# Performance work log

Measured on AMD Instinct MI355X. Metric: run time of the kernel, lower is better.

## Reference

```python
import jax, jax.numpy as jnp
import numpy as np

ALPHA = 0.2  # LeakyReLU negative slope
B, N, F_IN, F_OUT = 8, 2048, 256, 64


def setup_inputs() -> dict:
    key = jax.random.key(0)
    k1, k2, k3, k4 = jax.random.split(key, 4)
    x = jax.random.normal(k1, (B, N, F_IN), dtype=jnp.float32)
    adj = jax.random.randint(k2, (B, N, N), 0, 2, dtype=jnp.int32)
    # xavier_uniform with gain=1.414
    gain = 1.414
    lim_W = gain * np.sqrt(6.0 / (F_IN + F_OUT))
    W = jax.random.uniform(k3, (F_IN, F_OUT), dtype=jnp.float32, minval=-lim_W, maxval=lim_W)
    lim_a = gain * np.sqrt(6.0 / (2 * F_OUT + 1))
    a = jax.random.uniform(k4, (2 * F_OUT, 1), dtype=jnp.float32, minval=-lim_a, maxval=lim_a)
    return {"x": x, "adj": adj, "W": W, "a": a}


def reference(x, adj, W, a):
    h = jnp.einsum('bni,io->bno', x, W)  # [B, N, F_OUT]
    f_out = W.shape[1]
    # additive score a^T [h_i ; h_j] = (h_i . a_left) + (h_j . a_right)
    a_left = a[:f_out, 0]   # [F_OUT]
    a_right = a[f_out:, 0]  # [F_OUT]
    e_l = h @ a_left   # [B, N]
    e_r = h @ a_right  # [B, N]
    e = e_l[:, :, None] + e_r[:, None, :]          # [B, N, N]
    e = jnp.where(e > 0, e, ALPHA * e)             # LeakyReLU
    e = jnp.where(adj > 0, e, jnp.float32(-9e15))  # adjacency mask
    attention = jax.nn.softmax(e, axis=2)          # [B, N, N]
    h_prime = jnp.einsum('bnm,bmo->bno', attention, h)  # [B, N, F_OUT]
    return jax.nn.elu(h_prime)
```

## Files before the change

### kernel.cpp

```cpp
#include <hip/hip_runtime.h>
#include <math.h>

#define BATCH 8
#define NN 2048
#define FIN 256
#define FOUT 64
#define ALPHA 0.2f

typedef __attribute__((ext_vector_type(8))) short bf16x8;
typedef __attribute__((ext_vector_type(4))) float f32x4;

static __device__ __forceinline__ unsigned short f2bf(float f) {
  unsigned int u = __float_as_uint(f);
  u += 0x7fffu + ((u >> 16) & 1u);
  return (unsigned short)(u >> 16);
}
static __device__ __forceinline__ float bf2f(unsigned short h) {
  return __uint_as_float(((unsigned int)h) << 16);
}

__global__ __launch_bounds__(256) void k1_h(
    const float* __restrict__ x, const float* __restrict__ W,
    const float* __restrict__ a, float* __restrict__ el,
    float* __restrict__ er, unsigned char* __restrict__ hS) {
  __shared__ __align__(16) unsigned short lds[32768];
  const int t = threadIdx.x;
  const int wv = t >> 6;
  const int l = t & 63;
  const int l15 = l & 15;
  const int kg = l >> 4;

  {
    const float4* W4 = (const float4*)W;
    #pragma unroll
    for (int i = 0; i < 16; ++i) {
      int f = t + i * 256;
      float4 v = W4[f];
      int k = f >> 4;
      int ob = (f & 15) * 4;
      float vv[4] = {v.x, v.y, v.z, v.w};
      #pragma unroll
      for (int c = 0; c < 4; ++c) {
        int o = ob + c;
        unsigned short hi = f2bf(vv[c]);
        unsigned short lo = f2bf(vv[c] - bf2f(hi));
        int idx = o * 256 + (((k >> 3) ^ (o & 7)) * 8) + (k & 7);
        lds[idx] = hi;
        lds[16384 + idx] = lo;
      }
    }
  }
  __syncthreads();

  const int row = blockIdx.x * 64 + wv * 16 + l15;
  f32x4 acc[4] = {{0.f,0.f,0.f,0.f},{0.f,0.f,0.f,0.f},
                  {0.f,0.f,0.f,0.f},{0.f,0.f,0.f,0.f}};
  const float* xrow = x + (size_t)row * FIN;

  #pragma unroll
  for (int ks = 0; ks < 8; ++ks) {
    int k0 = ks * 32;
    float4 xa = *(const float4*)(xrow + k0 + kg * 8);
    float4 xb = *(const float4*)(xrow + k0 + kg * 8 + 4);
    float xv[8] = {xa.x, xa.y, xa.z, xa.w, xb.x, xb.y, xb.z, xb.w};
    bf16x8 ahi, alo;
    #pragma unroll
    for (int j = 0; j < 8; ++j) {
      unsigned short hi = f2bf(xv[j]);
      unsigned short lo = f2bf(xv[j] - bf2f(hi));
      ahi[j] = (short)hi;
      alo[j] = (short)lo;
    }
    int kgidx = ks * 4 + kg;
    #pragma unroll
    for (int ot = 0; ot < 4; ++ot) {
      int o = ot * 16 + l15;
      int base = o * 256 + ((kgidx ^ (o & 7)) * 8);
      bf16x8 bhi = *(const bf16x8*)&lds[base];
      bf16x8 blo = *(const bf16x8*)&lds[16384 + base];
      acc[ot] = __builtin_amdgcn_mfma_f32_16x16x32_bf16(ahi, bhi, acc[ot], 0, 0, 0);
      acc[ot] = __builtin_amdgcn_mfma_f32_16x16x32_bf16(ahi, blo, acc[ot], 0, 0, 0);
      acc[ot] = __builtin_amdgcn_mfma_f32_16x16x32_bf16(alo, bhi, acc[ot], 0, 0, 0);
    }
  }

  float aLv[4], aRv[4];
  #pragma unroll
  for (int ot = 0; ot < 4; ++ot) {
    aLv[ot] = a[ot * 16 + l15];
    aRv[ot] = a[64 + ot * 16 + l15];
  }
  #pragma unroll
  for (int jj = 0; jj < 4; ++jj) {
    float pl = 0.f, pr = 0.f;
    #pragma unroll
    for (int ot = 0; ot < 4; ++ot) {
      pl += acc[ot][jj] * aLv[ot];
      pr += acc[ot][jj] * aRv[ot];
    }
    #pragma unroll
    for (int s = 1; s < 16; s <<= 1) {
      pl += __shfl_xor(pl, s);
      pr += __shfl_xor(pr, s);
    }
    if (l15 == 0) {
      int grow = blockIdx.x * 64 + wv * 16 + kg * 4 + jj;
      el[grow] = pl;
      er[grow] = pr;
    }
  }

  __syncthreads();
  #pragma unroll
  for (int ot = 0; ot < 4; ++ot) {
    int o = ot * 16 + l15;
    int xorv = (o >> 1) & 3;
    #pragma unroll
    for (int jj = 0; jj < 4; ++jj) {
      int m_loc = wv * 16 + kg * 4 + jj;
      int ks2 = m_loc >> 5;
      int kg2 = (m_loc >> 3) & 3;
      int j = m_loc & 7;
      int kgp = kg2 ^ xorv;
      float v = acc[ot][jj];
      unsigned short hi = f2bf(v);
      unsigned short lo = f2bf(v - bf2f(hi));
      int base = ((ks2 * 2 + 0) * 64 + o) * 32 + kgp * 8 + j;
      lds[base] = hi;
      lds[base + 2048] = lo;
    }
  }
  __syncthreads();

  {
    const uint4* src = (const uint4*)(const void*)lds;
    uint4* dst = (uint4*)(hS + (size_t)blockIdx.x * 16384);
    #pragma unroll
    for (int i = 0; i < 4; ++i) dst[t + i * 256] = src[t + i * 256];
  }
}

__global__ __launch_bounds__(256, 3) void k2_attn(
    const int* __restrict__ adj, const unsigned char* __restrict__ hS,
    const float* __restrict__ el, const float* __restrict__ er,
    float* __restrict__ out) {
  __shared__ __align__(16) float cb[3 * 64 * 20];
  const int t = threadIdx.x;
  const int wv = t >> 6;
  const int l = t & 63;
  const int l15 = l & 15;
  const int kg = l >> 4;

  int bid = blockIdx.x;
  int swz = (bid & 7) * 128 + (bid >> 3);
  int b = swz >> 7;
  int n0 = (swz & 127) * 16;

  const int row = n0 + l15;
  const float eL = el[b * NN + row];
  const int* arow = adj + (size_t)b * NN * NN + (size_t)row * NN + wv * 512;
  const float* erp = er + b * NN + wv * 512;
  const unsigned char* hW = hS + (size_t)b * 32 * 16384 + (size_t)wv * 16 * 8192;
  const int laneoff = l15 * 64 + ((kg ^ ((l >> 1) & 3)) * 16);

  f32x4 acc[4] = {{0.f,0.f,0.f,0.f},{0.f,0.f,0.f,0.f},
                  {0.f,0.f,0.f,0.f},{0.f,0.f,0.f,0.f}};
  float S = 0.f;

  int4 av[3][2];
  float4 evc0, evc1, evn0, evn1;

  av[0][0] = *(const int4*)(arow + kg * 8);
  av[0][1] = *(const int4*)(arow + kg * 8 + 4);
  av[1][0] = *(const int4*)(arow + 32 + kg * 8);
  av[1][1] = *(const int4*)(arow + 32 + kg * 8 + 4);
  evc0 = *(const float4*)(erp + kg * 8);
  evc1 = *(const float4*)(erp + kg * 8 + 4);

  #pragma unroll
  for (int c = 0; c < 16; ++c) {
    bf16x8 curH[4], curL[4];
    {
      const unsigned char* p_ = hW + (size_t)c * 8192 + laneoff;
      #pragma unroll
      for (int ot = 0; ot < 4; ++ot) {
        curH[ot] = *(const bf16x8*)(p_ + ot * 1024);
        curL[ot] = *(const bf16x8*)(p_ + ot * 1024 + 4096);
      }
    }
    if (c < 14) {
      int mb = (c + 2) * 32;
      av[(c + 2) % 3][0] = *(const int4*)(arow + mb + kg * 8);
      av[(c + 2) % 3][1] = *(const int4*)(arow + mb + kg * 8 + 4);
    }
    if (c < 15) {
      evn0 = *(const float4*)(erp + (c + 1) * 32 + kg * 8);
      evn1 = *(const float4*)(erp + (c + 1) * 32 + kg * 8 + 4);
    }

    const int sl = c % 3;
    int a0[8] = {av[sl][0].x, av[sl][0].y, av[sl][0].z, av[sl][0].w,
                 av[sl][1].x, av[sl][1].y, av[sl][1].z, av[sl][1].w};
    float ee[8] = {evc0.x, evc0.y, evc0.z, evc0.w,
                   evc1.x, evc1.y, evc1.z, evc1.w};

    bf16x8 afh, afl;
    #pragma unroll
    for (int j = 0; j < 8; ++j) {
      float e0 = eL + ee[j];
      e0 = fmaxf(e0, ALPHA * e0);
      float w0 = (a0[j] > 0) ? __expf(e0) : 0.f;
      unsigned short h0 = f2bf(w0);
      float w0h = bf2f(h0);
      unsigned short l0 = f2bf(w0 - w0h);
      afh[j] = (short)h0;
      afl[j] = (short)l0;
      S += w0h + bf2f(l0);
    }

    #pragma unroll
    for (int ot = 0; ot < 4; ++ot) {
      acc[ot] = __builtin_amdgcn_mfma_f32_16x16x32_bf16(afh, curH[ot], acc[ot], 0, 0, 0);
      acc[ot] = __builtin_amdgcn_mfma_f32_16x16x32_bf16(afh, curL[ot], acc[ot], 0, 0, 0);
      acc[ot] = __builtin_amdgcn_mfma_f32_16x16x32_bf16(afl, curH[ot], acc[ot], 0, 0, 0);
    }

    if (c < 15) { evc0 = evn0; evc1 = evn1; }
  }

  S += __shfl_xor(S, 16);
  S += __shfl_xor(S, 32);

  __syncthreads();
  if (wv > 0) {
    float* dst = cb + ((wv - 1) * 64 + l) * 20;
    #pragma unroll
    for (int ot = 0; ot < 4; ++ot) *(f32x4*)(dst + ot * 4) = acc[ot];
    dst[16] = S;
  }
  __syncthreads();
  if (wv != 0) return;

  #pragma unroll
  for (int p = 0; p < 3; ++p) {
    const float* src = cb + (p * 64 + l) * 20;
    #pragma unroll
    for (int ot = 0; ot < 4; ++ot) acc[ot] += *(const f32x4*)(src + ot * 4);
    S += src[16];
  }

  float Sj[4];
  #pragma unroll
  for (int jj = 0; jj < 4; ++jj) Sj[jj] = __shfl(S, kg * 4 + jj);
  #pragma unroll
  for (int ot = 0; ot < 4; ++ot) {
    #pragma unroll
    for (int jj = 0; jj < 4; ++jj) {
      float v = acc[ot][jj] / Sj[jj];
      float r = v > 0.f ? v : expm1f(v);
      out[((size_t)b * NN + n0 + kg * 4 + jj) * FOUT + ot * 16 + l15] = r;
    }
  }
}

extern "C" void kernel_launch(void* const* d_in, const int* in_sizes, int n_in,
                              void* d_out, int out_size, void* d_ws, size_t ws_size,
                              hipStream_t stream) {
  const float* x   = (const float*)d_in[0];
  const int*   adj = (const int*)d_in[1];
  const float* W   = (const float*)d_in[2];
  const float* a   = (const float*)d_in[3];
  float* out = (float*)d_out;

  unsigned char* hS = (unsigned char*)d_ws;
  float* el = (float*)(hS + (size_t)BATCH * 32 * 16384);
  float* er = el + BATCH * NN;

  hipLaunchKernelGGL(k1_h, dim3(256), dim3(256), 0, stream, x, W, a, el, er, hS);
  hipLaunchKernelGGL(k2_attn, dim3(1024), dim3(256), 0, stream, adj, hS, el, er, out);
}
```

Baseline: 57.12 us.

## Warp-specialize attention kernel with producer wave streaming adjacency into LDS ring

The attention kernel is restructured so that each block covers 32 rows with two consumer waves that walk the full key dimension. A third producer wave streams the adjacency tiles into a 4-slot LDS ring using direct global-to-LDS loads, with block barriers each chunk to keep the waves in step. This replaces the old split-K design, which had four waves each taking a quarter of the keys and then reducing their partial results through LDS. The first kernel also swizzles its block order. The change is meant to overlap the adjacency HBM stream with the compute. In exchange it adds a per-chunk barrier and gives fewer waves per CU, which may lower the in-flight memory traffic.

```diff
diff --git a/kernel.cpp b/kernel.cpp
--- a/kernel.cpp
+++ b/kernel.cpp
@@ -6,6 +6,7 @@
 #define FIN 256
 #define FOUT 64
 #define ALPHA 0.2f
+#define RING 4
 
 typedef __attribute__((ext_vector_type(8))) short bf16x8;
 typedef __attribute__((ext_vector_type(4))) float f32x4;
@@ -17,6 +18,11 @@
 }
 static __device__ __forceinline__ float bf2f(unsigned short h) {
   return __uint_as_float(((unsigned int)h) << 16);
+}
+static __device__ __forceinline__ void gload16(const void* g, void* l) {
+  __builtin_amdgcn_global_load_lds(
+      (const __attribute__((address_space(1))) unsigned int*)g,
+      (__attribute__((address_space(3))) unsigned int*)l, 16, 0, 0);
 }
 
 __global__ __launch_bounds__(256) void k1_h(
@@ -29,6 +35,7 @@
   const int l = t & 63;
   const int l15 = l & 15;
   const int kg = l >> 4;
+  const int swz = (blockIdx.x & 7) * 32 + (blockIdx.x >> 3);
 
   {
     const float4* W4 = (const float4*)W;
@@ -52,7 +59,7 @@
   }
   __syncthreads();
 
-  const int row = blockIdx.x * 64 + wv * 16 + l15;
+  const int row = swz * 64 + wv * 16 + l15;
   f32x4 acc[4] = {{0.f,0.f,0.f,0.f},{0.f,0.f,0.f,0.f},
                   {0.f,0.f,0.f,0.f},{0.f,0.f,0.f,0.f}};
   const float* xrow = x + (size_t)row * FIN;
@@ -104,7 +111,7 @@
       pr += __shfl_xor(pr, s);
     }
     if (l15 == 0) {
-      int grow = blockIdx.x * 64 + wv * 16 + kg * 4 + jj;
+      int grow = swz * 64 + wv * 16 + kg * 4 + jj;
       el[grow] = pl;
       er[grow] = pr;
     }
@@ -134,121 +141,130 @@
 
   {
     const uint4* src = (const uint4*)(const void*)lds;
-    uint4* dst = (uint4*)(hS + (size_t)blockIdx.x * 16384);
+    uint4* dst = (uint4*)(hS + (size_t)swz * 16384);
     #pragma unroll
     for (int i = 0; i < 4; ++i) dst[t + i * 256] = src[t + i * 256];
   }
 }
 
-__global__ __launch_bounds__(256, 3) void k2_attn(
+__global__ __launch_bounds__(192, 2) void k2_attn(
     const int* __restrict__ adj, const unsigned char* __restrict__ hS,
     const float* __restrict__ el, const float* __restrict__ er,
     float* __restrict__ out) {
-  __shared__ __align__(16) float cb[3 * 64 * 20];
+  __shared__ __align__(1024) unsigned char ring[RING][32][128];
   const int t = threadIdx.x;
-  const int wv = t >> 6;
+  const int wv = t / 64;
   const int l = t & 63;
   const int l15 = l & 15;
   const int kg = l >> 4;
 
   int bid = blockIdx.x;
-  int swz = (bid & 7) * 128 + (bid >> 3);
-  int b = swz >> 7;
-  int n0 = (swz & 127) * 16;
-
-  const int row = n0 + l15;
-  const float eL = el[b * NN + row];
-  const int* arow = adj + (size_t)b * NN * NN + (size_t)row * NN + wv * 512;
-  const float* erp = er + b * NN + wv * 512;
-  const unsigned char* hW = hS + (size_t)b * 32 * 16384 + (size_t)wv * 16 * 8192;
+  int swz = (bid & 7) * 64 + (bid >> 3);
+  int b = swz >> 6;
+  int nb = (swz & 63) * 32;
+
+  const size_t adjBase = (size_t)b * NN * NN + (size_t)nb * NN;
+
+  if (wv == 2) {
+    const int r8 = l >> 3;
+    const int u  = l & 7;
+#define FILL(cc) {                                                          \
+      int slot_ = (cc) & (RING - 1);                                        \
+      _Pragma("unroll")                                                     \
+      for (int i_ = 0; i_ < 4; ++i_) {                                      \
+        int r_ = i_ * 8 + r8;                                               \
+        const unsigned char* src_ = (const unsigned char*)adj               \
+            + (adjBase + (size_t)r_ * NN + (size_t)(cc) * 32) * 4           \
+            + ((u ^ (r_ & 7)) << 4);                                        \
+        gload16(src_, &ring[slot_][i_ * 8][0]);                             \
+      } }
+    FILL(0); FILL(1); FILL(2);
+    asm volatile("s_waitcnt vmcnt(8)" ::: "memory");
+    __builtin_amdgcn_sched_barrier(0);
+    __builtin_amdgcn_s_barrier();
+    #pragma unroll 1
+    for (int c = 0; c < 64; ++c) {
+      if (c < 61) {
+        FILL(c + 3);
+        asm volatile("s_waitcnt vmcnt(8)" ::: "memory");
+      } else if (c == 61) {
+        asm volatile("s_waitcnt vmcnt(4)" ::: "memory");
+      } else if (c == 62) {
+        asm volatile("s_waitcnt vmcnt(0)" ::: "memory");
+      }
+      __builtin_amdgcn_sched_barrier(0);
+      __builtin_amdgcn_s_barrier();
+      asm volatile("" ::: "memory");
+    }
+#undef FILL
+    return;
+  }
+
+  const int r = wv * 16 + l15;
+  const float eL = el[b * NN + nb + r];
+  const float* erp = er + b * NN;
+  const unsigned char* hB = hS + (size_t)b * 32 * 16384;
   const int laneoff = l15 * 64 + ((kg ^ ((l >> 1) & 3)) * 16);
+  const int u0 = (kg * 2) ^ (l15 & 7);
+  const int u1 = (kg * 2 + 1) ^ (l15 & 7);
+  const int aoff0 = r * 128 + u0 * 16;
+  const int aoff1 = r * 128 + u1 * 16;
 
   f32x4 acc[4] = {{0.f,0.f,0.f,0.f},{0.f,0.f,0.f,0.f},
                   {0.f,0.f,0.f,0.f},{0.f,0.f,0.f,0.f}};
   float S = 0.f;
 
-  int4 av[3][2];
-  float4 evc0, evc1, evn0, evn1;
-
-  av[0][0] = *(const int4*)(arow + kg * 8);
-  av[0][1] = *(const int4*)(arow + kg * 8 + 4);
-  av[1][0] = *(const int4*)(arow + 32 + kg * 8);
-  av[1][1] = *(const int4*)(arow + 32 + kg * 8 + 4);
-  evc0 = *(const float4*)(erp + kg * 8);
-  evc1 = *(const float4*)(erp + kg * 8 + 4);
-
-  #pragma unroll
-  for (int c = 0; c < 16; ++c) {
-    bf16x8 curH[4], curL[4];
+  __builtin_amdgcn_s_barrier();
+  asm volatile("" ::: "memory");
+
+  #pragma unroll 1
+  for (int c = 0; c < 64; ++c) {
+    float4 e0 = *(const float4*)(erp + c * 32 + kg * 8);
+    float4 e1 = *(const float4*)(erp + c * 32 + kg * 8 + 4);
+    bf16x8 BH[4], BL[4];
     {
-      const unsigned char* p_ = hW + (size_t)c * 8192 + laneoff;
+      const unsigned char* p = hB + (size_t)c * 8192 + laneoff;
       #pragma unroll
       for (int ot = 0; ot < 4; ++ot) {
-        curH[ot] = *(const bf16x8*)(p_ + ot * 1024);
-        curL[ot] = *(const bf16x8*)(p_ + ot * 1024 + 4096);
+        BH[ot] = *(const bf16x8*)(p + ot * 1024);
+        BL[ot] = *(const bf16x8*)(p + ot * 1024 + 4096);
       }
     }
-    if (c < 14) {
-      int mb = (c + 2) * 32;
-      av[(c + 2) % 3][0] = *(const int4*)(arow + mb + kg * 8);
-      av[(c + 2) % 3][1] = *(const int4*)(arow + mb + kg * 8 + 4);
-    }
-    if (c < 15) {
-      evn0 = *(const float4*)(erp + (c + 1) * 32 + kg * 8);
-      evn1 = *(const float4*)(erp + (c + 1) * 32 + kg * 8 + 4);
-    }
-
-    const int sl = c % 3;
-    int a0[8] = {av[sl][0].x, av[sl][0].y, av[sl][0].z, av[sl][0].w,
-                 av[sl][1].x, av[sl][1].y, av[sl][1].z, av[sl][1].w};
-    float ee[8] = {evc0.x, evc0.y, evc0.z, evc0.w,
-                   evc1.x, evc1.y, evc1.z, evc1.w};
+    const unsigned char* rs = &ring[c & (RING - 1)][0][0];
+    int4 av0 = *(const int4*)(rs + aoff0);
+    int4 av1 = *(const int4*)(rs + aoff1);
+
+    int a0[8] = {av0.x, av0.y, av0.z, av0.w, av1.x, av1.y, av1.z, av1.w};
+    float ee[8] = {e0.x, e0.y, e0.z, e0.w, e1.x, e1.y, e1.z, e1.w};
 
     bf16x8 afh, afl;
     #pragma unroll
     for (int j = 0; j < 8; ++j) {
-      float e0 = eL + ee[j];
-      e0 = fmaxf(e0, ALPHA * e0);
-      float w0 = (a0[j] > 0) ? __expf(e0) : 0.f;
-      unsigned short h0 = f2bf(w0);
-      float w0h = bf2f(h0);
-      unsigned short l0 = f2bf(w0 - w0h);
-      afh[j] = (short)h0;
-      afl[j] = (short)l0;
-      S += w0h + bf2f(l0);
+      float e = eL + ee[j];
+      e = fmaxf(e, ALPHA * e);
+      float w = (a0[j] > 0) ? __expf(e) : 0.f;
+      unsigned short h = f2bf(w);
+      float wh = bf2f(h);
+      unsigned short lo = f2bf(w - wh);
+      afh[j] = (short)h;
+      afl[j] = (short)lo;
+      S += w;
     }
 
     #pragma unroll
     for (int ot = 0; ot < 4; ++ot) {
-      acc[ot] = __builtin_amdgcn_mfma_f32_16x16x32_bf16(afh, curH[ot], acc[ot], 0, 0, 0);
-      acc[ot] = __builtin_amdgcn_mfma_f32_16x16x32_bf16(afh, curL[ot], acc[ot], 0, 0, 0);
-      acc[ot] = __builtin_amdgcn_mfma_f32_16x16x32_bf16(afl, curH[ot], acc[ot], 0, 0, 0);
-    }
-
-    if (c < 15) { evc0 = evn0; evc1 = evn1; }
+      acc[ot] = __builtin_amdgcn_mfma_f32_16x16x32_bf16(afh, BH[ot], acc[ot], 0, 0, 0);
+      acc[ot] = __builtin_amdgcn_mfma_f32_16x16x32_bf16(afh, BL[ot], acc[ot], 0, 0, 0);
+      acc[ot] = __builtin_amdgcn_mfma_f32_16x16x32_bf16(afl, BH[ot], acc[ot], 0, 0, 0);
+    }
+
+    __builtin_amdgcn_sched_barrier(0);
+    __builtin_amdgcn_s_barrier();
+    asm volatile("" ::: "memory");
   }
 
   S += __shfl_xor(S, 16);
   S += __shfl_xor(S, 32);
-
-  __syncthreads();
-  if (wv > 0) {
-    float* dst = cb + ((wv - 1) * 64 + l) * 20;
-    #pragma unroll
-    for (int ot = 0; ot < 4; ++ot) *(f32x4*)(dst + ot * 4) = acc[ot];
-    dst[16] = S;
-  }
-  __syncthreads();
-  if (wv != 0) return;
-
-  #pragma unroll
-  for (int p = 0; p < 3; ++p) {
-    const float* src = cb + (p * 64 + l) * 20;
-    #pragma unroll
-    for (int ot = 0; ot < 4; ++ot) acc[ot] += *(const f32x4*)(src + ot * 4);
-    S += src[16];
-  }
-
   float Sj[4];
   #pragma unroll
   for (int jj = 0; jj < 4; ++jj) Sj[jj] = __shfl(S, kg * 4 + jj);
@@ -257,8 +273,8 @@
     #pragma unroll
     for (int jj = 0; jj < 4; ++jj) {
       float v = acc[ot][jj] / Sj[jj];
-      float r = v > 0.f ? v : expm1f(v);
-      out[((size_t)b * NN + n0 + kg * 4 + jj) * FOUT + ot * 16 + l15] = r;
+      float rr = v > 0.f ? v : expm1f(v);
+      out[((size_t)b * NN + nb + wv * 16 + kg * 4 + jj) * FOUT + ot * 16 + l15] = rr;
     }
   }
 }
@@ -277,5 +293,5 @@
   float* er = el + BATCH * NN;
 
   hipLaunchKernelGGL(k1_h, dim3(256), dim3(256), 0, stream, x, W, a, el, er, hS);
-  hipLaunchKernelGGL(k2_attn, dim3(1024), dim3(256), 0, stream, adj, hS, el, er, out);
-}
+  hipLaunchKernelGGL(k2_attn, dim3(512), dim3(192), 0, stream, adj, hS, el, er, out);
+}
```

Result: slower. 72.77 us (+27.4%).
